# Kernel optimization log

Hardware: AMD Instinct MI355X
Metric: run time of the kernel (lower is better)

## Reference

```python
import jax, jax.numpy as jnp
import numpy as np

# (multiplicity, l) segments, ir_mul layout: each segment stored as (2l+1, mul)
IRREPS = [(256, 0), (256, 1), (256, 2), (256, 3)]
BATCH = 8192
DIM = sum(m * (2 * l + 1) for m, l in IRREPS)  # 4096


def _real_basis_U(l):
    """Unitary change of basis from complex to real spherical harmonics (degree l)."""
    n = 2 * l + 1
    U = np.zeros((n, n), dtype=np.complex128)
    U[l, l] = 1.0
    s = 1.0 / np.sqrt(2.0)
    for mu in range(1, l + 1):
        U[l + mu, l - mu] = s
        U[l + mu, l + mu] = s * (-1.0) ** mu
        U[l - mu, l - mu] = 1j * s
        U[l - mu, l + mu] = -1j * s * (-1.0) ** mu
    return U


def _x_generator_eig(l):
    """Eigendecomposition (constants) of the x-axis angular-momentum operator in the real basis."""
    m = np.arange(-l, l + 1)
    n = 2 * l + 1
    Jp = np.zeros((n, n), dtype=np.complex128)
    mm = m[:-1]
    Jp[np.arange(1, n), np.arange(0, n - 1)] = np.sqrt(l * (l + 1) - mm * (mm + 1))
    Jx = (Jp + Jp.conj().T) / 2.0
    U = _real_basis_U(l)
    Jx_r = U @ Jx @ U.conj().T  # Hermitian
    w, V = np.linalg.eigh(Jx_r)  # w = -l..l (integers), V unitary
    return w, V


def _y_rotation(theta, l):
    """Rotation about y in the real irrep basis, built directly from the angle
    encoding [cos(l t),...,cos(t),1,sin(t),...,sin(l t)] -- diag cos(m t), antidiag +/- sin(m t)."""
    B = theta.shape[0]
    n = 2 * l + 1
    mu = jnp.arange(1, l + 1, dtype=theta.dtype)
    c = jnp.cos(mu * theta[:, None])  # [B, l]
    s = jnp.sin(mu * theta[:, None])  # [B, l]
    one = jnp.ones((B, 1), theta.dtype)
    zero = jnp.zeros((B, 1), theta.dtype)
    diag = jnp.concatenate([c[:, ::-1], one, c], axis=-1)    # [B, n]
    anti = jnp.concatenate([-s[:, ::-1], zero, s], axis=-1)  # [B, n]
    idx = jnp.arange(n)
    R = jnp.zeros((B, n, n), theta.dtype)
    R = R.at[:, idx, idx].set(diag)
    R = R.at[:, idx, idx[::-1]].add(anti)
    return R


def _x_rotation(theta, l, dtype):
    """Rotation about x: X(t) = Re(V diag(exp(-i t w)) V^H), done in real arithmetic."""
    w, V = _x_generator_eig(l)
    w = jnp.asarray(w, dtype)
    Vr = jnp.asarray(np.ascontiguousarray(V.real), dtype)
    Vi = jnp.asarray(np.ascontiguousarray(V.imag), dtype)
    C = jnp.cos(theta[:, None] * w)  # [B, n]
    S = jnp.sin(theta[:, None] * w)  # [B, n]
    X = (jnp.einsum('ik,bk,jk->bij', Vr, C, Vr)
         + jnp.einsum('ik,bk,jk->bij', Vi, C, Vi)
         + jnp.einsum('ik,bk,jk->bij', Vi, S, Vr)
         - jnp.einsum('ik,bk,jk->bij', Vr, S, Vi))
    return X


def _rotate(gamma, beta, alpha, x):
    # yxy Euler rotation: first gamma about y, then beta about x, then alpha about y.
    outs = []
    off = 0
    for mul, l in IRREPS:
        n = 2 * l + 1
        seg = x[:, off:off + n * mul].reshape(-1, n, mul)  # ir_mul layout
        D = _y_rotation(alpha, l) @ _x_rotation(beta, l, x.dtype) @ _y_rotation(gamma, l)
        outs.append(jnp.einsum('bij,bjm->bim', D, seg).reshape(-1, n * mul))
        off += n * mul
    return jnp.concatenate(outs, axis=-1)


def setup_inputs() -> dict:
    key = jax.random.key(0)
    kg, kb, ka, kx = jax.random.split(key, 4)
    return {
        'gamma': jax.random.normal(kg, (BATCH,), jnp.float32),
        'beta': jax.random.normal(kb, (BATCH,), jnp.float32),
        'alpha': jax.random.normal(ka, (BATCH,), jnp.float32),
        'x': jax.random.normal(kx, (BATCH, DIM), jnp.float32),
    }


def reference(gamma, beta, alpha, x):
    return _rotate(gamma, beta, alpha, x)
```

## Files before the change

kernel.cpp:

```cpp
#include <hip/hip_runtime.h>
#include <math.h>

#define BATCH 8192
#define DIM 4096


struct FT { float v[495]; };

constexpr double csqrt(double x) {
  double g = x > 1.0 ? x : 1.0;
  for (int i = 0; i < 50; ++i) g = 0.5 * (g + x / g);
  return g;
}

constexpr void mmc(int n, const double* A, const double* B, double* C) {
  for (int i = 0; i < n; ++i)
    for (int j = 0; j < n; ++j) {
      double s = 0.0;
      for (int k = 0; k < n; ++k) s += A[i * n + k] * B[k * n + j];
      C[i * n + j] = s;
    }
}

constexpr FT compute_ft() {
  FT o{};
  for (int l = 1; l <= 3; ++l) {
    const int n = 2 * l + 1, nn = n * n;
    double JX[49] = {}, UR[49] = {}, UI[49] = {};
    for (int a = 0; a < n - 1; ++a) {
      double m = (double)(a - l);
      double v = 0.5 * csqrt((double)(l * (l + 1)) - m * (m + 1.0));
      JX[(a + 1) * n + a] = v;
      JX[a * n + (a + 1)] = v;
    }
    UR[l * n + l] = 1.0;
    const double s = csqrt(0.5);
    for (int mu = 1; mu <= l; ++mu) {
      double sg = (mu & 1) ? -1.0 : 1.0;
      UR[(l + mu) * n + (l - mu)] = s;
      UR[(l + mu) * n + (l + mu)] = s * sg;
      UI[(l - mu) * n + (l - mu)] = s;
      UI[(l - mu) * n + (l + mu)] = -s * sg;
    }
    double MR[49] = {}, MI[49] = {};
    mmc(n, UR, JX, MR);
    mmc(n, UI, JX, MI);
    double K[49] = {};
    for (int a = 0; a < n; ++a)
      for (int b = 0; b < n; ++b) {
        double acc = 0.0;
        for (int c = 0; c < n; ++c)
          acc += MI[a * n + c] * UR[b * n + c] - MR[a * n + c] * UI[b * n + c];
        K[a * n + b] = acc;
      }
    const double TH = 0.78539816339744830962;
    double S[49] = {}, P[49] = {}, T[49] = {};
    for (int i = 0; i < nn; ++i) S[i] = K[i] * (TH / 16.0);
    for (int i = 0; i < n; ++i) P[i * n + i] = 1.0;
    for (int t = 12; t >= 1; --t) {
      mmc(n, S, P, T);
      double inv = 1.0 / (double)t;
      for (int i = 0; i < nn; ++i) P[i] = T[i] * inv;
      for (int i = 0; i < n; ++i) P[i * n + i] += 1.0;
    }
    for (int q = 0; q < 4; ++q) {
      mmc(n, P, P, T);
      for (int i = 0; i < nn; ++i) P[i] = T[i];
    }
    double acc[7][49] = {};
    double Ek[49] = {}, Et[49] = {};
    for (int i = 0; i < n; ++i) Ek[i * n + i] = 1.0;
    const double r2 = csqrt(0.5);
    const double c8[8] = {1.0, r2, 0.0, -r2, -1.0, -r2, 0.0, r2};
    const double s8[8] = {0.0, r2, 1.0, r2, 0.0, -r2, -1.0, -r2};
    for (int k = 0; k < 8; ++k) {
      for (int i = 0; i < nn; ++i) acc[0][i] += 0.125 * Ek[i];
      for (int mu = 1; mu <= l; ++mu) {
        int a8 = (mu * k) & 7;
        double cc = 0.25 * c8[a8], ss = 0.25 * s8[a8];
        for (int i = 0; i < nn; ++i) {
          acc[2 * mu - 1][i] += cc * Ek[i];
          acc[2 * mu][i] += ss * Ek[i];
        }
      }
      mmc(n, Ek, P, Et);
      for (int i = 0; i < nn; ++i) Ek[i] = Et[i];
    }
    int base = (l == 1) ? 0 : ((l == 2) ? 27 : 152);
    for (int t = 0; t <= 2 * l; ++t)
      for (int i = 0; i < nn; ++i) o.v[base + t * nn + i] = (float)acc[t][i];
  }
  return o;
}

__device__ __constant__ FT c_tb = compute_ft();

typedef float vf4 __attribute__((ext_vector_type(4)));

__device__ __forceinline__ vf4 vfma4(float a, vf4 v, vf4 acc) { return acc + a * v; }

__device__ __forceinline__ float entry_for(int e, float cb1, float cb2, float cb3,
                                           float sb1, float sb2, float sb3,
                                           float al, float ga) {
  int l, n, basec, i, j;
  if (e < 9)       { l = 1; n = 3; basec = 0;   int r = e;      i = r / 3; j = r - i * 3; }
  else if (e < 34) { l = 2; n = 5; basec = 27;  int r = e - 9;  i = r / 5; j = r - i * 5; }
  else             { l = 3; n = 7; basec = 152; int r = e - 34; i = r / 7; j = r - i * 7; }

  const float* C = c_tb.v + basec;
  const int ip = n - 1 - i, jp = n - 1 - j;
  const int nn = n * n;
  float xij = 0.f, xijp = 0.f, xipj = 0.f, xipjp = 0.f;
  #pragma unroll
  for (int tt = 0; tt < 7; ++tt) {
    if (tt <= 2 * l) {
      float coef;
      if (tt == 0) coef = 1.f;
      else if (tt == 1) coef = cb1;
      else if (tt == 2) coef = sb1;
      else if (tt == 3) coef = cb2;
      else if (tt == 4) coef = sb2;
      else if (tt == 5) coef = cb3;
      else coef = sb3;
      const float* M = C + tt * nn;
      xij   = fmaf(coef, M[i * n + j],   xij);
      xijp  = fmaf(coef, M[i * n + jp],  xijp);
      xipj  = fmaf(coef, M[ip * n + j],  xipj);
      xipjp = fmaf(coef, M[ip * n + jp], xipjp);
    }
  }
  float sa, ca, sg, cg;
  sincosf((float)(i - l) * al, &sa, &ca);
  sincosf((float)(j - l) * ga, &sg, &cg);
  return (ca * xij + sa * xipj) * cg - (ca * xijp + sa * xipjp) * sg;
}

__device__ __forceinline__ float dget(float d0, float d1, int e) {
  float s = (e < 64) ? d0 : d1;
  return __builtin_bit_cast(
      float, __builtin_amdgcn_readlane(__builtin_bit_cast(int, s), e & 63));
}

__global__ __launch_bounds__(256) void rot_wave(
    const float* __restrict__ gamma, const float* __restrict__ beta,
    const float* __restrict__ alpha, const float* __restrict__ x,
    float* __restrict__ out) {
  const int tid = threadIdx.x;
  const int lane = tid & 63;
  const int wv = tid >> 6;
  const size_t b = (size_t)blockIdx.x * 4 + wv;
  const vf4* __restrict__ xin = (const vf4*)x + b * 1024;
  vf4* __restrict__ xo = (vf4*)out + b * 1024;

  vf4 v0 = xin[lane];
  vf4 v1[3], v2[5], v3[7];
  #pragma unroll
  for (int j = 0; j < 3; ++j) v1[j] = xin[64 + j * 64 + lane];
  #pragma unroll
  for (int j = 0; j < 5; ++j) v2[j] = xin[256 + j * 64 + lane];
  #pragma unroll
  for (int j = 0; j < 7; ++j) v3[j] = xin[576 + j * 64 + lane];
  asm volatile("" ::"v"(v0), "v"(v1[0]), "v"(v1[1]), "v"(v1[2]), "v"(v2[0]),
               "v"(v2[1]), "v"(v2[2]), "v"(v2[3]), "v"(v2[4]), "v"(v3[0]),
               "v"(v3[1]), "v"(v3[2]), "v"(v3[3]), "v"(v3[4]), "v"(v3[5]),
               "v"(v3[6]));

  const float al = alpha[b], bt = beta[b], ga = gamma[b];
  float cb1, sb1;
  sincosf(bt, &sb1, &cb1);
  const float cb2 = cb1 * cb1 - sb1 * sb1, sb2 = 2.f * sb1 * cb1;
  const float cb3 = cb2 * cb1 - sb2 * sb1, sb3 = sb2 * cb1 + cb2 * sb1;

  const float d0 = entry_for(lane, cb1, cb2, cb3, sb1, sb2, sb3, al, ga);
  int e2 = lane + 64;
  if (e2 > 82) e2 = 82;
  const float d1 = entry_for(e2, cb1, cb2, cb3, sb1, sb2, sb3, al, ga);

  __builtin_nontemporal_store(v0, &xo[lane]);

  #pragma unroll
  for (int i = 0; i < 3; ++i) {
    vf4 o = (vf4)(0.f);
    #pragma unroll
    for (int j = 0; j < 3; ++j) o = vfma4(dget(d0, d1, i * 3 + j), v1[j], o);
    __builtin_nontemporal_store(o, &xo[64 + i * 64 + lane]);
  }
  #pragma unroll
  for (int i = 0; i < 5; ++i) {
    vf4 o = (vf4)(0.f);
    #pragma unroll
    for (int j = 0; j < 5; ++j) o = vfma4(dget(d0, d1, 9 + i * 5 + j), v2[j], o);
    __builtin_nontemporal_store(o, &xo[256 + i * 64 + lane]);
  }
  #pragma unroll
  for (int i = 0; i < 7; ++i) {
    vf4 o = (vf4)(0.f);
    #pragma unroll
    for (int j = 0; j < 7; ++j) o = vfma4(dget(d0, d1, 34 + i * 7 + j), v3[j], o);
    __builtin_nontemporal_store(o, &xo[576 + i * 64 + lane]);
  }
}

extern "C" void kernel_launch(void* const* d_in, const int* in_sizes, int n_in,
                              void* d_out, int out_size, void* d_ws, size_t ws_size,
                              hipStream_t stream) {
  const float* gamma = (const float*)d_in[0];
  const float* beta  = (const float*)d_in[1];
  const float* alpha = (const float*)d_in[2];
  const float* x     = (const float*)d_in[3];
  float* out = (float*)d_out;

  rot_wave<<<BATCH / 4, 256, 0, stream>>>(gamma, beta, alpha, x, out);
}
```

Measured before the change: 49.38 us.

## Process two batch rows per wave, prefetching second row during first compute

```diff
diff --git a/kernel.cpp b/kernel.cpp
--- a/kernel.cpp
+++ b/kernel.cpp
@@ -141,63 +141,109 @@
       float, __builtin_amdgcn_readlane(__builtin_bit_cast(int, s), e & 63));
 }
 
-__global__ __launch_bounds__(256) void rot_wave(
+#define PIN16(v0, v1, v2, v3)                                                  \
+  asm volatile("" ::"v"(v0), "v"(v1[0]), "v"(v1[1]), "v"(v1[2]), "v"(v2[0]),   \
+               "v"(v2[1]), "v"(v2[2]), "v"(v2[3]), "v"(v2[4]), "v"(v3[0]),     \
+               "v"(v3[1]), "v"(v3[2]), "v"(v3[3]), "v"(v3[4]), "v"(v3[5]),     \
+               "v"(v3[6]))
+
+__global__ __launch_bounds__(256) void rot_pipe(
     const float* __restrict__ gamma, const float* __restrict__ beta,
     const float* __restrict__ alpha, const float* __restrict__ x,
     float* __restrict__ out) {
   const int tid = threadIdx.x;
   const int lane = tid & 63;
   const int wv = tid >> 6;
-  const size_t b = (size_t)blockIdx.x * 4 + wv;
-  const vf4* __restrict__ xin = (const vf4*)x + b * 1024;
-  vf4* __restrict__ xo = (vf4*)out + b * 1024;
-
-  vf4 v0 = xin[lane];
-  vf4 v1[3], v2[5], v3[7];
-  #pragma unroll
-  for (int j = 0; j < 3; ++j) v1[j] = xin[64 + j * 64 + lane];
-  #pragma unroll
-  for (int j = 0; j < 5; ++j) v2[j] = xin[256 + j * 64 + lane];
-  #pragma unroll
-  for (int j = 0; j < 7; ++j) v3[j] = xin[576 + j * 64 + lane];
-  asm volatile("" ::"v"(v0), "v"(v1[0]), "v"(v1[1]), "v"(v1[2]), "v"(v2[0]),
-               "v"(v2[1]), "v"(v2[2]), "v"(v2[3]), "v"(v2[4]), "v"(v3[0]),
-               "v"(v3[1]), "v"(v3[2]), "v"(v3[3]), "v"(v3[4]), "v"(v3[5]),
-               "v"(v3[6]));
-
-  const float al = alpha[b], bt = beta[b], ga = gamma[b];
+  const size_t bA = (size_t)blockIdx.x * 4 + wv;
+  const size_t bB = bA + BATCH / 2;
+
+  const float alA = alpha[bA], btA = beta[bA], gaA = gamma[bA];
+  const float alB = alpha[bB], btB = beta[bB], gaB = gamma[bB];
+
+  const vf4* __restrict__ xinA = (const vf4*)x + bA * 1024;
+  const vf4* __restrict__ xinB = (const vf4*)x + bB * 1024;
+  vf4* __restrict__ xoA = (vf4*)out + bA * 1024;
+  vf4* __restrict__ xoB = (vf4*)out + bB * 1024;
+
+  vf4 a0 = xinA[lane];
+  vf4 a1[3], a2[5], a3[7];
+  #pragma unroll
+  for (int j = 0; j < 3; ++j) a1[j] = xinA[64 + j * 64 + lane];
+  #pragma unroll
+  for (int j = 0; j < 5; ++j) a2[j] = xinA[256 + j * 64 + lane];
+  #pragma unroll
+  for (int j = 0; j < 7; ++j) a3[j] = xinA[576 + j * 64 + lane];
+  PIN16(a0, a1, a2, a3);
+
   float cb1, sb1;
-  sincosf(bt, &sb1, &cb1);
-  const float cb2 = cb1 * cb1 - sb1 * sb1, sb2 = 2.f * sb1 * cb1;
-  const float cb3 = cb2 * cb1 - sb2 * sb1, sb3 = sb2 * cb1 + cb2 * sb1;
-
-  const float d0 = entry_for(lane, cb1, cb2, cb3, sb1, sb2, sb3, al, ga);
+  sincosf(btA, &sb1, &cb1);
+  float cb2 = cb1 * cb1 - sb1 * sb1, sb2 = 2.f * sb1 * cb1;
+  float cb3 = cb2 * cb1 - sb2 * sb1, sb3 = sb2 * cb1 + cb2 * sb1;
+  const float d0A = entry_for(lane, cb1, cb2, cb3, sb1, sb2, sb3, alA, gaA);
   int e2 = lane + 64;
   if (e2 > 82) e2 = 82;
-  const float d1 = entry_for(e2, cb1, cb2, cb3, sb1, sb2, sb3, al, ga);
-
-  __builtin_nontemporal_store(v0, &xo[lane]);
-
+  const float d1A = entry_for(e2, cb1, cb2, cb3, sb1, sb2, sb3, alA, gaA);
+
+  vf4 q0 = xinB[lane];
+  vf4 q1[3], q2[5], q3[7];
+  #pragma unroll
+  for (int j = 0; j < 3; ++j) q1[j] = xinB[64 + j * 64 + lane];
+  #pragma unroll
+  for (int j = 0; j < 5; ++j) q2[j] = xinB[256 + j * 64 + lane];
+  #pragma unroll
+  for (int j = 0; j < 7; ++j) q3[j] = xinB[576 + j * 64 + lane];
+  PIN16(q0, q1, q2, q3);
+
+  __builtin_nontemporal_store(a0, &xoA[lane]);
   #pragma unroll
   for (int i = 0; i < 3; ++i) {
     vf4 o = (vf4)(0.f);
     #pragma unroll
-    for (int j = 0; j < 3; ++j) o = vfma4(dget(d0, d1, i * 3 + j), v1[j], o);
-    __builtin_nontemporal_store(o, &xo[64 + i * 64 + lane]);
+    for (int j = 0; j < 3; ++j) o = vfma4(dget(d0A, d1A, i * 3 + j), a1[j], o);
+    __builtin_nontemporal_store(o, &xoA[64 + i * 64 + lane]);
   }
   #pragma unroll
   for (int i = 0; i < 5; ++i) {
     vf4 o = (vf4)(0.f);
     #pragma unroll
-    for (int j = 0; j < 5; ++j) o = vfma4(dget(d0, d1, 9 + i * 5 + j), v2[j], o);
-    __builtin_nontemporal_store(o, &xo[256 + i * 64 + lane]);
+    for (int j = 0; j < 5; ++j) o = vfma4(dget(d0A, d1A, 9 + i * 5 + j), a2[j], o);
+    __builtin_nontemporal_store(o, &xoA[256 + i * 64 + lane]);
   }
   #pragma unroll
   for (int i = 0; i < 7; ++i) {
     vf4 o = (vf4)(0.f);
     #pragma unroll
-    for (int j = 0; j < 7; ++j) o = vfma4(dget(d0, d1, 34 + i * 7 + j), v3[j], o);
-    __builtin_nontemporal_store(o, &xo[576 + i * 64 + lane]);
+    for (int j = 0; j < 7; ++j) o = vfma4(dget(d0A, d1A, 34 + i * 7 + j), a3[j], o);
+    __builtin_nontemporal_store(o, &xoA[576 + i * 64 + lane]);
+  }
+
+  sincosf(btB, &sb1, &cb1);
+  cb2 = cb1 * cb1 - sb1 * sb1; sb2 = 2.f * sb1 * cb1;
+  cb3 = cb2 * cb1 - sb2 * sb1; sb3 = sb2 * cb1 + cb2 * sb1;
+  const float d0B = entry_for(lane, cb1, cb2, cb3, sb1, sb2, sb3, alB, gaB);
+  const float d1B = entry_for(e2, cb1, cb2, cb3, sb1, sb2, sb3, alB, gaB);
+
+  __builtin_nontemporal_store(q0, &xoB[lane]);
+  #pragma unroll
+  for (int i = 0; i < 3; ++i) {
+    vf4 o = (vf4)(0.f);
+    #pragma unroll
+    for (int j = 0; j < 3; ++j) o = vfma4(dget(d0B, d1B, i * 3 + j), q1[j], o);
+    __builtin_nontemporal_store(o, &xoB[64 + i * 64 + lane]);
+  }
+  #pragma unroll
+  for (int i = 0; i < 5; ++i) {
+    vf4 o = (vf4)(0.f);
+    #pragma unroll
+    for (int j = 0; j < 5; ++j) o = vfma4(dget(d0B, d1B, 9 + i * 5 + j), q2[j], o);
+    __builtin_nontemporal_store(o, &xoB[256 + i * 64 + lane]);
+  }
+  #pragma unroll
+  for (int i = 0; i < 7; ++i) {
+    vf4 o = (vf4)(0.f);
+    #pragma unroll
+    for (int j = 0; j < 7; ++j) o = vfma4(dget(d0B, d1B, 34 + i * 7 + j), q3[j], o);
+    __builtin_nontemporal_store(o, &xoB[576 + i * 64 + lane]);
   }
 }
 
@@ -210,5 +256,5 @@
   const float* x     = (const float*)d_in[3];
   float* out = (float*)d_out;
 
-  rot_wave<<<BATCH / 4, 256, 0, stream>>>(gamma, beta, alpha, x, out);
-}
+  rot_pipe<<<BATCH / 8, 256, 0, stream>>>(gamma, beta, alpha, x, out);
+}
```

After: 48.03 us. 2.7% less time.

## Split each batch row across three waves, one per irrep degree

Applied to the files above, without the earlier changes.

```diff
diff --git a/kernel.cpp b/kernel.cpp
--- a/kernel.cpp
+++ b/kernel.cpp
@@ -135,69 +135,85 @@
   return (ca * xij + sa * xipj) * cg - (ca * xijp + sa * xipjp) * sg;
 }
 
-__device__ __forceinline__ float dget(float d0, float d1, int e) {
-  float s = (e < 64) ? d0 : d1;
+__device__ __forceinline__ float dget1(float d, int k) {
   return __builtin_bit_cast(
-      float, __builtin_amdgcn_readlane(__builtin_bit_cast(int, s), e & 63));
-}
-
-__global__ __launch_bounds__(256) void rot_wave(
+      float, __builtin_amdgcn_readlane(__builtin_bit_cast(int, d), k));
+}
+
+__global__ __launch_bounds__(192) void rot_seg(
     const float* __restrict__ gamma, const float* __restrict__ beta,
     const float* __restrict__ alpha, const float* __restrict__ x,
     float* __restrict__ out) {
   const int tid = threadIdx.x;
   const int lane = tid & 63;
   const int wv = tid >> 6;
-  const size_t b = (size_t)blockIdx.x * 4 + wv;
+  const size_t b = (size_t)blockIdx.x;
   const vf4* __restrict__ xin = (const vf4*)x + b * 1024;
   vf4* __restrict__ xo = (vf4*)out + b * 1024;
 
-  vf4 v0 = xin[lane];
-  vf4 v1[3], v2[5], v3[7];
-  #pragma unroll
-  for (int j = 0; j < 3; ++j) v1[j] = xin[64 + j * 64 + lane];
-  #pragma unroll
-  for (int j = 0; j < 5; ++j) v2[j] = xin[256 + j * 64 + lane];
-  #pragma unroll
-  for (int j = 0; j < 7; ++j) v3[j] = xin[576 + j * 64 + lane];
-  asm volatile("" ::"v"(v0), "v"(v1[0]), "v"(v1[1]), "v"(v1[2]), "v"(v2[0]),
-               "v"(v2[1]), "v"(v2[2]), "v"(v2[3]), "v"(v2[4]), "v"(v3[0]),
-               "v"(v3[1]), "v"(v3[2]), "v"(v3[3]), "v"(v3[4]), "v"(v3[5]),
-               "v"(v3[6]));
-
   const float al = alpha[b], bt = beta[b], ga = gamma[b];
-  float cb1, sb1;
-  sincosf(bt, &sb1, &cb1);
-  const float cb2 = cb1 * cb1 - sb1 * sb1, sb2 = 2.f * sb1 * cb1;
-  const float cb3 = cb2 * cb1 - sb2 * sb1, sb3 = sb2 * cb1 + cb2 * sb1;
-
-  const float d0 = entry_for(lane, cb1, cb2, cb3, sb1, sb2, sb3, al, ga);
-  int e2 = lane + 64;
-  if (e2 > 82) e2 = 82;
-  const float d1 = entry_for(e2, cb1, cb2, cb3, sb1, sb2, sb3, al, ga);
-
-  __builtin_nontemporal_store(v0, &xo[lane]);
-
-  #pragma unroll
-  for (int i = 0; i < 3; ++i) {
-    vf4 o = (vf4)(0.f);
-    #pragma unroll
-    for (int j = 0; j < 3; ++j) o = vfma4(dget(d0, d1, i * 3 + j), v1[j], o);
-    __builtin_nontemporal_store(o, &xo[64 + i * 64 + lane]);
-  }
-  #pragma unroll
-  for (int i = 0; i < 5; ++i) {
-    vf4 o = (vf4)(0.f);
-    #pragma unroll
-    for (int j = 0; j < 5; ++j) o = vfma4(dget(d0, d1, 9 + i * 5 + j), v2[j], o);
-    __builtin_nontemporal_store(o, &xo[256 + i * 64 + lane]);
-  }
-  #pragma unroll
-  for (int i = 0; i < 7; ++i) {
-    vf4 o = (vf4)(0.f);
-    #pragma unroll
-    for (int j = 0; j < 7; ++j) o = vfma4(dget(d0, d1, 34 + i * 7 + j), v3[j], o);
-    __builtin_nontemporal_store(o, &xo[576 + i * 64 + lane]);
+
+  if (wv == 0) {
+    vf4 v0 = xin[lane];
+    vf4 v1[3];
+    #pragma unroll
+    for (int j = 0; j < 3; ++j) v1[j] = xin[64 + j * 64 + lane];
+    asm volatile("" ::"v"(v0), "v"(v1[0]), "v"(v1[1]), "v"(v1[2]));
+
+    float cb1, sb1;
+    sincosf(bt, &sb1, &cb1);
+    int e = lane < 9 ? lane : 8;
+    const float d = entry_for(e, cb1, 0.f, 0.f, sb1, 0.f, 0.f, al, ga);
+
+    __builtin_nontemporal_store(v0, &xo[lane]);
+    #pragma unroll
+    for (int i = 0; i < 3; ++i) {
+      vf4 o = (vf4)(0.f);
+      #pragma unroll
+      for (int j = 0; j < 3; ++j) o = vfma4(dget1(d, i * 3 + j), v1[j], o);
+      __builtin_nontemporal_store(o, &xo[64 + i * 64 + lane]);
+    }
+  } else if (wv == 1) {
+    vf4 v2[5];
+    #pragma unroll
+    for (int j = 0; j < 5; ++j) v2[j] = xin[256 + j * 64 + lane];
+    asm volatile("" ::"v"(v2[0]), "v"(v2[1]), "v"(v2[2]), "v"(v2[3]),
+                 "v"(v2[4]));
+
+    float cb1, sb1;
+    sincosf(bt, &sb1, &cb1);
+    const float cb2 = cb1 * cb1 - sb1 * sb1, sb2 = 2.f * sb1 * cb1;
+    int e = 9 + (lane < 25 ? lane : 24);
+    const float d = entry_for(e, cb1, cb2, 0.f, sb1, sb2, 0.f, al, ga);
+
+    #pragma unroll
+    for (int i = 0; i < 5; ++i) {
+      vf4 o = (vf4)(0.f);
+      #pragma unroll
+      for (int j = 0; j < 5; ++j) o = vfma4(dget1(d, i * 5 + j), v2[j], o);
+      __builtin_nontemporal_store(o, &xo[256 + i * 64 + lane]);
+    }
+  } else {
+    vf4 v3[7];
+    #pragma unroll
+    for (int j = 0; j < 7; ++j) v3[j] = xin[576 + j * 64 + lane];
+    asm volatile("" ::"v"(v3[0]), "v"(v3[1]), "v"(v3[2]), "v"(v3[3]),
+                 "v"(v3[4]), "v"(v3[5]), "v"(v3[6]));
+
+    float cb1, sb1;
+    sincosf(bt, &sb1, &cb1);
+    const float cb2 = cb1 * cb1 - sb1 * sb1, sb2 = 2.f * sb1 * cb1;
+    const float cb3 = cb2 * cb1 - sb2 * sb1, sb3 = sb2 * cb1 + cb2 * sb1;
+    int e = 34 + (lane < 49 ? lane : 48);
+    const float d = entry_for(e, cb1, cb2, cb3, sb1, sb2, sb3, al, ga);
+
+    #pragma unroll
+    for (int i = 0; i < 7; ++i) {
+      vf4 o = (vf4)(0.f);
+      #pragma unroll
+      for (int j = 0; j < 7; ++j) o = vfma4(dget1(d, i * 7 + j), v3[j], o);
+      __builtin_nontemporal_store(o, &xo[576 + i * 64 + lane]);
+    }
   }
 }
 
@@ -210,5 +226,5 @@
   const float* x     = (const float*)d_in[3];
   float* out = (float*)d_out;
 
-  rot_wave<<<BATCH / 4, 256, 0, stream>>>(gamma, beta, alpha, x, out);
-}
+  rot_seg<<<BATCH, 192, 0, stream>>>(gamma, beta, alpha, x, out);
+}
```

New measurement: 43.99 us. 10.9% less time.
